# Optimization experiments

Measured on AMD Instinct MI355X. Metric: run time of the kernel, lower is better.

## Reference

```python
import jax, jax.numpy as jnp
import numpy as np
from jax.scipy.special import erf

# synthetic covalent radii table (original imports `covalent_radii`, e.g. from ase)
COV_RADII = jnp.asarray(0.3 + 0.02 * np.arange(100), dtype=jnp.float32)

B_MOL = 1024   # molecules per batch
N_ATOM = 128   # atoms per molecule (equal-sized ragged batch, atoms sorted by molecule)
N_ELEM = 10


def setup_inputs() -> dict:
    key = jax.random.key(0)
    ks = jax.random.split(key, 6)
    N = B_MOL * N_ATOM
    return {
        "eneg": jax.random.normal(ks[0], (N, 1), jnp.float32),
        "positions": jax.random.normal(ks[1], (N, 3), jnp.float32) * 3.0,
        "node_attrs": jax.random.uniform(ks[2], (N, N_ELEM), jnp.float32),
        "hardness": jax.random.uniform(ks[3], (N_ELEM,), jnp.float32),
        "total_charge": jax.random.normal(ks[4], (B_MOL,), jnp.float32),
        "batch": jnp.repeat(jnp.arange(B_MOL), N_ATOM),          # sorted molecule ids
        "atomic_numbers": jax.random.randint(ks[5], (N,), 1, 90),
    }


def reference(eneg, positions, node_attrs, hardness, total_charge, batch, atomic_numbers):
    # atoms are sorted by molecule with equal molecule sizes, so the ragged
    # python loop of the original collapses to a batched [B, n, ...] computation.
    B = total_charge.shape[0]
    N = positions.shape[0]
    n = N // B
    sqrt_pi = jnp.sqrt(jnp.asarray(np.pi, jnp.float32))
    sqrt_2 = jnp.sqrt(jnp.asarray(2.0, jnp.float32))

    pos = positions.reshape(B, n, 3)
    Z = atomic_numbers.reshape(B, n)
    atom_idx = jnp.argmax(node_attrs, axis=1).reshape(B, n)

    r = COV_RADII[Z]                                     # [B, n]
    diag_vals = hardness[atom_idx] + 1.0 / (sqrt_pi * r)  # [B, n]
    sigma = jnp.square(r)                                # [B, n]
    gamma = jnp.sqrt(sigma[:, :, None] + sigma[:, None, :])  # [B, n, n]

    diff = pos[:, :, None, :] - pos[:, None, :, :]       # [B, n, n, 3]
    sq = jnp.sum(diff * diff, axis=-1)                   # [B, n, n]
    eye = jnp.eye(n, dtype=bool)
    dist = jnp.sqrt(jnp.where(eye, 1.0, sq))             # safe diag (overwritten below)

    A = erf(dist / (sqrt_2 * gamma)) / dist              # [B, n, n]
    A = jnp.where(eye, diag_vals[:, :, None], A)         # scatter hardness diagonal

    # augment with charge-conservation row/column of ones (corner = 1)
    A = jnp.concatenate([A, jnp.ones((B, n, 1), A.dtype)], axis=2)
    A = jnp.concatenate([A, jnp.ones((B, 1, n + 1), A.dtype)], axis=1)

    b = jnp.concatenate([-eneg.reshape(B, n, 1),
                         total_charge.reshape(B, 1, 1)], axis=1)  # [B, n+1, 1]

    x = jnp.linalg.solve(A, b)                           # batched small solves
    return x[:, :n, 0].reshape(-1)                       # partial charges, [N]
```

## Files before the change

kernel.cpp:

```cpp
#include <hip/hip_runtime.h>
#include <math.h>

#define NMOL  1024
#define N     128
#define NELEM 10
#define BLOCK 256
#define PW    8
#define NPAN  16
#define PSTR  12
#define USTR  132

typedef __attribute__((ext_vector_type(4))) float f4;


__global__ __launch_bounds__(BLOCK, 2) void ceq_solve_kernel(
    const float* __restrict__ eneg,
    const float* __restrict__ positions,
    const float* __restrict__ node_attrs,
    const float* __restrict__ hardness,
    const float* __restrict__ total_charge,
    const int*   __restrict__ atomic_numbers,
    float* __restrict__ out)
{
    __shared__ __align__(16) float P[2][N * PSTR];
    __shared__ __align__(16) float Up[2][PW * USTR];
    __shared__ __align__(16) float Ublk[2][NPAN][PW][PW];
    __shared__ float rhsY[2][N], rhsZ[2][N];
    __shared__ float sxY[2][N], sxZ[2][N];
    __shared__ float px[2][N], py[2][N], pz[2][N], sg[2][N], dgv[2][N];
    __shared__ float lamS[2];

    const int tid  = threadIdx.x;
    const int lane = tid & 63;
    const int wid  = tid >> 6;
    const int g    = tid >> 7;
    const int wv   = wid & 1;
    const int gt   = tid & 127;
    const int r0   = 2 * lane;
    const int r1   = r0 + 1;
    const int col0 = 64 * wv;
    const int mol  = 2 * blockIdx.x + g;
    const int base = mol * N;

    {
        const int i = gt;
        const int Z = atomic_numbers[base + i];
        const float rad = 0.3f + 0.02f * (float)Z;
        sg[g][i] = rad * rad;
        const float* na = node_attrs + (size_t)(base + i) * NELEM;
        float best = na[0]; int bi = 0;
        #pragma unroll
        for (int e = 1; e < NELEM; ++e) {
            float v = na[e];
            if (v > best) { best = v; bi = e; }
        }
        dgv[g][i] = hardness[bi] + 0.5641895835477563f / rad;
        const float* p = positions + (size_t)(base + i) * 3;
        px[g][i] = p[0]; py[g][i] = p[1]; pz[g][i] = p[2];
        rhsY[g][i] = -eneg[base + i];
        rhsZ[g][i] = 1.0f;
    }
    __syncthreads();

    f4 Ar0[16], Ar1[16];
    {
        const float x0 = px[g][r0], y0 = py[g][r0], z0 = pz[g][r0];
        const float s0 = sg[g][r0], d0 = dgv[g][r0];
        #pragma unroll
        for (int c = 0; c < 16; ++c) {
            f4 v0;
            #pragma unroll
            for (int e = 0; e < 4; ++e) {
                const int j = col0 + 4 * c + e;
                float a0;
                if (j == r0) a0 = d0;
                else {
                    const float dx = x0 - px[g][j], dy = y0 - py[g][j], dz = z0 - pz[g][j];
                    const float d = sqrtf(dx * dx + dy * dy + dz * dz);
                    a0 = erff(d / (1.4142135623730951f * sqrtf(s0 + sg[g][j]))) / d;
                }
                ((float*)&v0)[e] = a0;
            }
            Ar0[c] = v0;
        }
        const float x1 = px[g][r1], y1 = py[g][r1], z1 = pz[g][r1];
        const float s1 = sg[g][r1], d1 = dgv[g][r1];
        #pragma unroll
        for (int c = 0; c < 16; ++c) {
            f4 v1;
            #pragma unroll
            for (int e = 0; e < 4; ++e) {
                const int j = col0 + 4 * c + e;
                float a1;
                if (j == r1) a1 = d1;
                else {
                    const float dx = x1 - px[g][j], dy = y1 - py[g][j], dz = z1 - pz[g][j];
                    const float d = sqrtf(dx * dx + dy * dy + dz * dz);
                    a1 = erff(d / (1.4142135623730951f * sqrtf(s1 + sg[g][j]))) / d;
                }
                ((float*)&v1)[e] = a1;
            }
            Ar1[c] = v1;
        }
    }

    for (int p = 0; p < NPAN; ++p) {
        const int k0   = PW * p;
        const int gclo = 2 * p + 2;
        const int q    = p & 7;

        if (wv == (p >> 3) && lane >= 4 * p) {
            f4 a00, a01, a10, a11;
            switch (q) {
                case 0:  a00 = Ar0[0];  a01 = Ar0[1];  a10 = Ar1[0];  a11 = Ar1[1];  break;
                case 1:  a00 = Ar0[2];  a01 = Ar0[3];  a10 = Ar1[2];  a11 = Ar1[3];  break;
                case 2:  a00 = Ar0[4];  a01 = Ar0[5];  a10 = Ar1[4];  a11 = Ar1[5];  break;
                case 3:  a00 = Ar0[6];  a01 = Ar0[7];  a10 = Ar1[6];  a11 = Ar1[7];  break;
                case 4:  a00 = Ar0[8];  a01 = Ar0[9];  a10 = Ar1[8];  a11 = Ar1[9];  break;
                case 5:  a00 = Ar0[10]; a01 = Ar0[11]; a10 = Ar1[10]; a11 = Ar1[11]; break;
                case 6:  a00 = Ar0[12]; a01 = Ar0[13]; a10 = Ar1[12]; a11 = Ar1[13]; break;
                default: a00 = Ar0[14]; a01 = Ar0[15]; a10 = Ar1[14]; a11 = Ar1[15]; break;
            }
            *(f4*)&P[g][r0 * PSTR + 0] = a00; *(f4*)&P[g][r0 * PSTR + 4] = a01;
            *(f4*)&P[g][r1 * PSTR + 0] = a10; *(f4*)&P[g][r1 * PSTR + 4] = a11;
        }
        if (gt < PW) {
            Up[g][gt * USTR + 128] = rhsY[g][k0 + gt];
            Up[g][gt * USTR + 129] = rhsZ[g][k0 + gt];
        }
        __syncthreads();

        if (wv == 0) {
            const int i0 = k0 + lane, i1 = i0 + 64;
            const bool v0 = i0 < N, v1 = i1 < N;
            float rg0[PW], rg1[PW];
            if (v0) {
                f4 a = *(const f4*)&P[g][i0 * PSTR], b = *(const f4*)&P[g][i0 * PSTR + 4];
                rg0[0]=a.x; rg0[1]=a.y; rg0[2]=a.z; rg0[3]=a.w;
                rg0[4]=b.x; rg0[5]=b.y; rg0[6]=b.z; rg0[7]=b.w;
            } else {
                #pragma unroll
                for (int j = 0; j < PW; ++j) rg0[j] = 0.0f;
            }
            if (v1) {
                f4 a = *(const f4*)&P[g][i1 * PSTR], b = *(const f4*)&P[g][i1 * PSTR + 4];
                rg1[0]=a.x; rg1[1]=a.y; rg1[2]=a.z; rg1[3]=a.w;
                rg1[4]=b.x; rg1[5]=b.y; rg1[6]=b.z; rg1[7]=b.w;
            } else {
                #pragma unroll
                for (int j = 0; j < PW; ++j) rg1[j] = 0.0f;
            }
            #pragma unroll
            for (int kk = 0; kk < PW; ++kk) {
                float pr[PW];
                #pragma unroll
                for (int j = kk; j < PW; ++j) pr[j] = __shfl(rg0[j], kk);
                const float dinv = 1.0f / pr[kk];
                if (v0 && i0 > k0 + kk) {
                    const float mult = rg0[kk] * dinv; rg0[kk] = mult;
                    #pragma unroll
                    for (int j = kk + 1; j < PW; ++j) rg0[j] -= mult * pr[j];
                }
                if (v0 && lane >= PW) Up[g][kk * USTR + i0] = rg0[kk] * pr[kk];
                if (v1) {
                    const float mult = rg1[kk] * dinv; rg1[kk] = mult;
                    #pragma unroll
                    for (int j = kk + 1; j < PW; ++j) rg1[j] -= mult * pr[j];
                    Up[g][kk * USTR + i1] = rg1[kk] * pr[kk];
                }
            }
            if (v0) {
                f4 a = { rg0[0], rg0[1], rg0[2], rg0[3] };
                f4 b = { rg0[4], rg0[5], rg0[6], rg0[7] };
                *(f4*)&P[g][i0 * PSTR] = a; *(f4*)&P[g][i0 * PSTR + 4] = b;
                if (lane < PW) {
                    *(f4*)&Ublk[g][p][lane][0] = a; *(f4*)&Ublk[g][p][lane][4] = b;
                }
            }
            if (v1) {
                f4 a = { rg1[0], rg1[1], rg1[2], rg1[3] };
                f4 b = { rg1[4], rg1[5], rg1[6], rg1[7] };
                *(f4*)&P[g][i1 * PSTR] = a; *(f4*)&P[g][i1 * PSTR + 4] = b;
            }
        }
        __syncthreads();

        if (gt < 2) {
            const int j = 128 + gt;
            float u[PW];
            #pragma unroll
            for (int kk = 0; kk < PW; ++kk) u[kk] = Up[g][kk * USTR + j];
            #pragma unroll
            for (int kk = 1; kk < PW; ++kk) {
                float acc = u[kk];
                #pragma unroll
                for (int t = 0; t < kk; ++t) acc -= Ublk[g][p][kk][t] * u[t];
                u[kk] = acc;
            }
            #pragma unroll
            for (int kk = 0; kk < PW; ++kk) Up[g][kk * USTR + j] = u[kk];
        }
        __syncthreads();

        if (lane >= 4 * p && lane < 4 * p + 4) {
            const int u0 = r0 - k0, u1 = u0 + 1;
            #pragma unroll
            for (int c = 0; c < 16; ++c) {
                const int gc = 16 * wv + c;
                if (gc >= gclo) {
                    Ar0[c] = *(const f4*)&Up[g][u0 * USTR + 4 * gc];
                    Ar1[c] = *(const f4*)&Up[g][u1 * USTR + 4 * gc];
                }
            }
        }
        if (gt < PW) {
            rhsY[g][k0 + gt] = Up[g][gt * USTR + 128];
            rhsZ[g][k0 + gt] = Up[g][gt * USTR + 129];
        }
        const bool hasmat = (16 * wv + 15) >= gclo;
        if (lane >= 4 * p + 4) {
            float lA0[PW], lA1[PW];
            if (hasmat || wv == 0) {
                f4 a = *(const f4*)&P[g][r0 * PSTR], b = *(const f4*)&P[g][r0 * PSTR + 4];
                lA0[0]=a.x; lA0[1]=a.y; lA0[2]=a.z; lA0[3]=a.w;
                lA0[4]=b.x; lA0[5]=b.y; lA0[6]=b.z; lA0[7]=b.w;
                f4 c2 = *(const f4*)&P[g][r1 * PSTR], d2 = *(const f4*)&P[g][r1 * PSTR + 4];
                lA1[0]=c2.x; lA1[1]=c2.y; lA1[2]=c2.z; lA1[3]=c2.w;
                lA1[4]=d2.x; lA1[5]=d2.y; lA1[6]=d2.z; lA1[7]=d2.w;
            }
            if (hasmat) {
                #pragma unroll
                for (int c = 0; c < 16; ++c) {
                    const int gc = 16 * wv + c;
                    if (gc >= gclo) {
                        f4 acc0 = Ar0[c], acc1 = Ar1[c];
                        #pragma unroll
                        for (int u = 0; u < PW; ++u) {
                            const f4 uv = *(const f4*)&Up[g][u * USTR + 4 * gc];
                            acc0 -= uv * lA0[u];
                            acc1 -= uv * lA1[u];
                        }
                        Ar0[c] = acc0; Ar1[c] = acc1;
                    }
                }
            }
            if (wv == 0) {
                float yy0 = rhsY[g][r0], yy1 = rhsY[g][r1];
                float zz0 = rhsZ[g][r0], zz1 = rhsZ[g][r1];
                #pragma unroll
                for (int u = 0; u < PW; ++u) {
                    const float uy = Up[g][u * USTR + 128];
                    const float uz = Up[g][u * USTR + 129];
                    yy0 -= lA0[u] * uy; yy1 -= lA1[u] * uy;
                    zz0 -= lA0[u] * uz; zz1 -= lA1[u] * uz;
                }
                rhsY[g][r0] = yy0; rhsY[g][r1] = yy1;
                rhsZ[g][r0] = zz0; rhsZ[g][r1] = zz1;
            }
        }
        __syncthreads();
    }

    for (int pb = NPAN - 1; pb >= 0; --pb) {
        const int k0 = PW * pb;
        if (tid < 4) {
            const int gg = tid >> 1;
            float* rhs = (tid & 1) ? rhsZ[gg] : rhsY[gg];
            float* sx  = (tid & 1) ? sxZ[gg]  : sxY[gg];
            float x[PW];
            #pragma unroll
            for (int kk = PW - 1; kk >= 0; --kk) {
                float acc = rhs[k0 + kk];
                #pragma unroll
                for (int jj = kk + 1; jj < PW; ++jj) acc -= Ublk[gg][pb][kk][jj] * x[jj];
                x[kk] = acc / Ublk[gg][pb][kk][kk];
                sx[k0 + kk] = x[kk];
            }
        }
        __syncthreads();
        if (wv == (pb >> 3) && lane < 4 * pb) {
            f4 a00, a01, a10, a11;
            switch (pb & 7) {
                case 0:  a00 = Ar0[0];  a01 = Ar0[1];  a10 = Ar1[0];  a11 = Ar1[1];  break;
                case 1:  a00 = Ar0[2];  a01 = Ar0[3];  a10 = Ar1[2];  a11 = Ar1[3];  break;
                case 2:  a00 = Ar0[4];  a01 = Ar0[5];  a10 = Ar1[4];  a11 = Ar1[5];  break;
                case 3:  a00 = Ar0[6];  a01 = Ar0[7];  a10 = Ar1[6];  a11 = Ar1[7];  break;
                case 4:  a00 = Ar0[8];  a01 = Ar0[9];  a10 = Ar1[8];  a11 = Ar1[9];  break;
                case 5:  a00 = Ar0[10]; a01 = Ar0[11]; a10 = Ar1[10]; a11 = Ar1[11]; break;
                case 6:  a00 = Ar0[12]; a01 = Ar0[13]; a10 = Ar1[12]; a11 = Ar1[13]; break;
                default: a00 = Ar0[14]; a01 = Ar0[15]; a10 = Ar1[14]; a11 = Ar1[15]; break;
            }
            float yy0 = rhsY[g][r0], yy1 = rhsY[g][r1];
            float zz0 = rhsZ[g][r0], zz1 = rhsZ[g][r1];
            yy0 -= a00.x*sxY[g][k0]   + a00.y*sxY[g][k0+1] + a00.z*sxY[g][k0+2] + a00.w*sxY[g][k0+3]
                 + a01.x*sxY[g][k0+4] + a01.y*sxY[g][k0+5] + a01.z*sxY[g][k0+6] + a01.w*sxY[g][k0+7];
            yy1 -= a10.x*sxY[g][k0]   + a10.y*sxY[g][k0+1] + a10.z*sxY[g][k0+2] + a10.w*sxY[g][k0+3]
                 + a11.x*sxY[g][k0+4] + a11.y*sxY[g][k0+5] + a11.z*sxY[g][k0+6] + a11.w*sxY[g][k0+7];
            zz0 -= a00.x*sxZ[g][k0]   + a00.y*sxZ[g][k0+1] + a00.z*sxZ[g][k0+2] + a00.w*sxZ[g][k0+3]
                 + a01.x*sxZ[g][k0+4] + a01.y*sxZ[g][k0+5] + a01.z*sxZ[g][k0+6] + a01.w*sxZ[g][k0+7];
            zz1 -= a10.x*sxZ[g][k0]   + a10.y*sxZ[g][k0+1] + a10.z*sxZ[g][k0+2] + a10.w*sxZ[g][k0+3]
                 + a11.x*sxZ[g][k0+4] + a11.y*sxZ[g][k0+5] + a11.z*sxZ[g][k0+6] + a11.w*sxZ[g][k0+7];
            rhsY[g][r0] = yy0; rhsY[g][r1] = yy1;
            rhsZ[g][r0] = zz0; rhsZ[g][r1] = zz1;
        }
        __syncthreads();
    }

    if (wv == 0) {
        float vY = sxY[g][lane] + sxY[g][lane + 64];
        float vZ = sxZ[g][lane] + sxZ[g][lane + 64];
        #pragma unroll
        for (int off = 32; off; off >>= 1) {
            vY += __shfl_xor(vY, off);
            vZ += __shfl_xor(vZ, off);
        }
        if (lane == 0) lamS[g] = (vY - total_charge[mol]) / (vZ - 1.0f);
    }
    __syncthreads();
    out[base + gt] = sxY[g][gt] - lamS[g] * sxZ[g][gt];
}

extern "C" void kernel_launch(void* const* d_in, const int* in_sizes, int n_in,
                              void* d_out, int out_size, void* d_ws, size_t ws_size,
                              hipStream_t stream) {
    const float* eneg           = (const float*)d_in[0];
    const float* positions      = (const float*)d_in[1];
    const float* node_attrs     = (const float*)d_in[2];
    const float* hardness       = (const float*)d_in[3];
    const float* total_charge   = (const float*)d_in[4];
    const int*   atomic_numbers = (const int*)d_in[6];
    float* out = (float*)d_out;

    ceq_solve_kernel<<<NMOL / 2, BLOCK, 0, stream>>>(
        eneg, positions, node_attrs, hardness, total_charge, atomic_numbers, out);
}
```

Baseline: 225.7 us.

## Fold RHS elimination into panel factorization and drop a barrier stage

The two right-hand-side vectors are now eliminated inside the wave-0 panel factorization loop. Pivot-row RHS values are broadcast via shuffles and updated alongside the L multipliers, which replaces the separate triangular solve on the Up staging columns and the later rhs update in the trailing step. This removes one __syncthreads per panel, the small serial forward-substitution by two threads, and the staging copies. In exchange wave 0 does a few more FMAs and shuffles per column step, and the trailing update is restricted to waves that own matrix columns.

```diff
diff --git a/kernel.cpp b/kernel.cpp
--- a/kernel.cpp
+++ b/kernel.cpp
@@ -124,48 +124,53 @@
             *(f4*)&P[g][r0 * PSTR + 0] = a00; *(f4*)&P[g][r0 * PSTR + 4] = a01;
             *(f4*)&P[g][r1 * PSTR + 0] = a10; *(f4*)&P[g][r1 * PSTR + 4] = a11;
         }
-        if (gt < PW) {
-            Up[g][gt * USTR + 128] = rhsY[g][k0 + gt];
-            Up[g][gt * USTR + 129] = rhsZ[g][k0 + gt];
-        }
         __syncthreads();
 
         if (wv == 0) {
             const int i0 = k0 + lane, i1 = i0 + 64;
             const bool v0 = i0 < N, v1 = i1 < N;
             float rg0[PW], rg1[PW];
+            float rY0, rZ0, rY1, rZ1;
             if (v0) {
                 f4 a = *(const f4*)&P[g][i0 * PSTR], b = *(const f4*)&P[g][i0 * PSTR + 4];
                 rg0[0]=a.x; rg0[1]=a.y; rg0[2]=a.z; rg0[3]=a.w;
                 rg0[4]=b.x; rg0[5]=b.y; rg0[6]=b.z; rg0[7]=b.w;
+                rY0 = rhsY[g][i0]; rZ0 = rhsZ[g][i0];
             } else {
                 #pragma unroll
                 for (int j = 0; j < PW; ++j) rg0[j] = 0.0f;
+                rY0 = 0.0f; rZ0 = 0.0f;
             }
             if (v1) {
                 f4 a = *(const f4*)&P[g][i1 * PSTR], b = *(const f4*)&P[g][i1 * PSTR + 4];
                 rg1[0]=a.x; rg1[1]=a.y; rg1[2]=a.z; rg1[3]=a.w;
                 rg1[4]=b.x; rg1[5]=b.y; rg1[6]=b.z; rg1[7]=b.w;
+                rY1 = rhsY[g][i1]; rZ1 = rhsZ[g][i1];
             } else {
                 #pragma unroll
                 for (int j = 0; j < PW; ++j) rg1[j] = 0.0f;
+                rY1 = 0.0f; rZ1 = 0.0f;
             }
             #pragma unroll
             for (int kk = 0; kk < PW; ++kk) {
                 float pr[PW];
                 #pragma unroll
                 for (int j = kk; j < PW; ++j) pr[j] = __shfl(rg0[j], kk);
+                const float cY = __shfl(rY0, kk);
+                const float cZ = __shfl(rZ0, kk);
                 const float dinv = 1.0f / pr[kk];
-                if (v0 && i0 > k0 + kk) {
+                if (v0 && lane > kk) {
                     const float mult = rg0[kk] * dinv; rg0[kk] = mult;
                     #pragma unroll
                     for (int j = kk + 1; j < PW; ++j) rg0[j] -= mult * pr[j];
+                    rY0 -= mult * cY; rZ0 -= mult * cZ;
                 }
                 if (v0 && lane >= PW) Up[g][kk * USTR + i0] = rg0[kk] * pr[kk];
                 if (v1) {
                     const float mult = rg1[kk] * dinv; rg1[kk] = mult;
                     #pragma unroll
                     for (int j = kk + 1; j < PW; ++j) rg1[j] -= mult * pr[j];
+                    rY1 -= mult * cY; rZ1 -= mult * cZ;
                     Up[g][kk * USTR + i1] = rg1[kk] * pr[kk];
                 }
             }
@@ -173,6 +178,7 @@
                 f4 a = { rg0[0], rg0[1], rg0[2], rg0[3] };
                 f4 b = { rg0[4], rg0[5], rg0[6], rg0[7] };
                 *(f4*)&P[g][i0 * PSTR] = a; *(f4*)&P[g][i0 * PSTR + 4] = b;
+                rhsY[g][i0] = rY0; rhsZ[g][i0] = rZ0;
                 if (lane < PW) {
                     *(f4*)&Ublk[g][p][lane][0] = a; *(f4*)&Ublk[g][p][lane][4] = b;
                 }
@@ -181,24 +187,8 @@
                 f4 a = { rg1[0], rg1[1], rg1[2], rg1[3] };
                 f4 b = { rg1[4], rg1[5], rg1[6], rg1[7] };
                 *(f4*)&P[g][i1 * PSTR] = a; *(f4*)&P[g][i1 * PSTR + 4] = b;
-            }
-        }
-        __syncthreads();
-
-        if (gt < 2) {
-            const int j = 128 + gt;
-            float u[PW];
-            #pragma unroll
-            for (int kk = 0; kk < PW; ++kk) u[kk] = Up[g][kk * USTR + j];
-            #pragma unroll
-            for (int kk = 1; kk < PW; ++kk) {
-                float acc = u[kk];
-                #pragma unroll
-                for (int t = 0; t < kk; ++t) acc -= Ublk[g][p][kk][t] * u[t];
-                u[kk] = acc;
-            }
-            #pragma unroll
-            for (int kk = 0; kk < PW; ++kk) Up[g][kk * USTR + j] = u[kk];
+                rhsY[g][i1] = rY1; rhsZ[g][i1] = rZ1;
+            }
         }
         __syncthreads();
 
@@ -213,14 +203,10 @@
                 }
             }
         }
-        if (gt < PW) {
-            rhsY[g][k0 + gt] = Up[g][gt * USTR + 128];
-            rhsZ[g][k0 + gt] = Up[g][gt * USTR + 129];
-        }
         const bool hasmat = (16 * wv + 15) >= gclo;
-        if (lane >= 4 * p + 4) {
+        if (hasmat && lane >= 4 * p + 4) {
             float lA0[PW], lA1[PW];
-            if (hasmat || wv == 0) {
+            {
                 f4 a = *(const f4*)&P[g][r0 * PSTR], b = *(const f4*)&P[g][r0 * PSTR + 4];
                 lA0[0]=a.x; lA0[1]=a.y; lA0[2]=a.z; lA0[3]=a.w;
                 lA0[4]=b.x; lA0[5]=b.y; lA0[6]=b.z; lA0[7]=b.w;
@@ -228,34 +214,19 @@
                 lA1[0]=c2.x; lA1[1]=c2.y; lA1[2]=c2.z; lA1[3]=c2.w;
                 lA1[4]=d2.x; lA1[5]=d2.y; lA1[6]=d2.z; lA1[7]=d2.w;
             }
-            if (hasmat) {
-                #pragma unroll
-                for (int c = 0; c < 16; ++c) {
-                    const int gc = 16 * wv + c;
-                    if (gc >= gclo) {
-                        f4 acc0 = Ar0[c], acc1 = Ar1[c];
-                        #pragma unroll
-                        for (int u = 0; u < PW; ++u) {
-                            const f4 uv = *(const f4*)&Up[g][u * USTR + 4 * gc];
-                            acc0 -= uv * lA0[u];
-                            acc1 -= uv * lA1[u];
-                        }
-                        Ar0[c] = acc0; Ar1[c] = acc1;
+            #pragma unroll
+            for (int c = 0; c < 16; ++c) {
+                const int gc = 16 * wv + c;
+                if (gc >= gclo) {
+                    f4 acc0 = Ar0[c], acc1 = Ar1[c];
+                    #pragma unroll
+                    for (int u = 0; u < PW; ++u) {
+                        const f4 uv = *(const f4*)&Up[g][u * USTR + 4 * gc];
+                        acc0 -= uv * lA0[u];
+                        acc1 -= uv * lA1[u];
                     }
-                }
-            }
-            if (wv == 0) {
-                float yy0 = rhsY[g][r0], yy1 = rhsY[g][r1];
-                float zz0 = rhsZ[g][r0], zz1 = rhsZ[g][r1];
-                #pragma unroll
-                for (int u = 0; u < PW; ++u) {
-                    const float uy = Up[g][u * USTR + 128];
-                    const float uz = Up[g][u * USTR + 129];
-                    yy0 -= lA0[u] * uy; yy1 -= lA1[u] * uy;
-                    zz0 -= lA0[u] * uz; zz1 -= lA1[u] * uz;
-                }
-                rhsY[g][r0] = yy0; rhsY[g][r1] = yy1;
-                rhsZ[g][r0] = zz0; rhsZ[g][r1] = zz1;
+                    Ar0[c] = acc0; Ar1[c] = acc1;
+                }
             }
         }
         __syncthreads();
```

Result: no change. 223.0 us (-1.2%).
